# Kernel tuning notes

Measured on AMD Instinct MI355X. Metric: run time of the kernel, lower is better.

Reference implementation:

```python
import jax, jax.numpy as jnp
import numpy as np

BETA = 0.25  # commitment loss weight


def setup_inputs() -> dict:
    key = jax.random.key(0)
    k1, k2 = jax.random.split(key)
    B, D, H, W = 16, 256, 64, 64
    K = 2048  # num_codebook
    z = jax.random.normal(k1, (B, D, H, W), dtype=jnp.float32)
    # matches nn.Embedding init uniform_(-1/K, 1/K) in scale-free way; values irrelevant to math
    codebook = jax.random.uniform(k2, (K, D), dtype=jnp.float32,
                                  minval=-1.0 / K, maxval=1.0 / K)
    return {"z": z, "codebook": codebook}


def reference(z, codebook):
    # z: (B, D, H, W) -> (B, H, W, D) -> (N, D)
    b, d, h, w = z.shape
    k = codebook.shape[0]
    z_flat = jnp.transpose(z, (0, 2, 3, 1)).reshape(-1, d)  # (N, D)

    # squared L2 distance via sum-of-squares + matmul (same expansion as torch code)
    distance = (jnp.sum(z_flat * z_flat, axis=1, keepdims=True)
                + jnp.sum(codebook * codebook, axis=1)
                - 2.0 * jnp.matmul(z_flat, codebook.T))  # (N, K)
    vq_indices = jnp.argmin(distance, axis=1)  # (N,)
    z_quantized = codebook[vq_indices]  # (N, D) gather

    # one-hot counting (scatter-add, equivalent to sum of one-hot)
    vq_current_count = jnp.zeros((k,), dtype=jnp.int32).at[vq_indices].add(1)

    sg = jax.lax.stop_gradient
    codebook_loss = jnp.mean((z_quantized - sg(z_flat)) ** 2)
    commitment_loss = jnp.mean((z_flat - sg(z_quantized)) ** 2)
    loss = codebook_loss + BETA * commitment_loss

    # straight-through estimator
    z_st = z_flat + sg(z_quantized - z_flat)
    q = jnp.transpose(z_st.reshape(b, h, w, d), (0, 3, 1, 2))  # (B, D, H, W)
    return q, loss, codebook_loss, commitment_loss, vq_current_count
```

## Files before the change

kernel.cpp:

```cpp
#include <hip/hip_runtime.h>

#define N_TOT 65536
#define K_CB  2048
#define D_DIM 256
#define HW    4096
#define DHW   1048576

typedef _Float16 half8 __attribute__((ext_vector_type(8)));
typedef _Float16 half4v __attribute__((ext_vector_type(4)));
typedef float f32x16 __attribute__((ext_vector_type(16)));


__device__ __forceinline__ void gload_lds16(const void* g, void* l) {
    __builtin_amdgcn_global_load_lds((const __attribute__((address_space(1))) void*)g,
                                     (__attribute__((address_space(3))) void*)l, 16, 0, 0);
}

__device__ __forceinline__ float pw128_sq(const float* __restrict__ base, int stride) {
    #pragma clang fp contract(off)
    float r[8];
    #pragma unroll
    for (int j = 0; j < 8; ++j) { float v = base[j * stride]; r[j] = v * v; }
    for (int i = 8; i < 128; i += 8) {
        #pragma unroll
        for (int j = 0; j < 8; ++j) { float v = base[(i + j) * stride]; r[j] += v * v; }
    }
    return ((r[0] + r[1]) + (r[2] + r[3])) + ((r[4] + r[5]) + (r[6] + r[7]));
}

__global__ void cbnorm_zero_kernel(const float* __restrict__ cb, float* __restrict__ cb2,
                                   int* __restrict__ counts, float* __restrict__ sse) {
    #pragma clang fp contract(off)
    int k = blockIdx.x * 256 + threadIdx.x;
    const float* row = cb + (size_t)k * D_DIM;
    cb2[k] = pw128_sq(row, 1) + pw128_sq(row + 128, 1);
    counts[k] = 0;
    if (k == 0) *sse = 0.f;
}

__global__ void split_c_kernel(const float* __restrict__ cb,
                               _Float16* __restrict__ ch, _Float16* __restrict__ cl) {
    int e = (blockIdx.x * 256 + threadIdx.x) * 4;
    float4 v = *(const float4*)(cb + e);
    float xs[4] = {v.x, v.y, v.z, v.w};
    half4v hh, hl;
    #pragma unroll
    for (int u = 0; u < 4; ++u) {
        float x = xs[u] * 16384.0f;
        _Float16 hv = (_Float16)x;
        hh[u] = hv;
        hl[u] = (_Float16)(x - (float)hv);
    }
    *(half4v*)(ch + e) = hh;
    *(half4v*)(cl + e) = hl;
}

__global__ void fused_z_kernel(const float* __restrict__ z,
                               _Float16* __restrict__ zh, _Float16* __restrict__ zl,
                               float* __restrict__ z2,
                               unsigned long long* __restrict__ rowmin_g) {
    __shared__ __align__(16) float lt[256 * 33];
    __shared__ float rj[512];
    __shared__ float hh[64];
    int t = threadIdx.x;
    int n0 = blockIdx.x * 32;
    int b = n0 >> 12, s0 = n0 & 4095;
    const float* zb = z + (size_t)b * DHW + s0;

    #pragma unroll
    for (int v = 0; v < 8; ++v) {
        int f = v * 256 + t;
        int d = f >> 3, nch = f & 7;
        float4 val = *(const float4*)(zb + (size_t)d * HW + nch * 4);
        lt[d * 33 + nch * 4 + 0] = val.x;
        lt[d * 33 + nch * 4 + 1] = val.y;
        lt[d * 33 + nch * 4 + 2] = val.z;
        lt[d * 33 + nch * 4 + 3] = val.w;
    }
    __syncthreads();

    {
        #pragma clang fp contract(off)
        int n = t & 31, j = t >> 5;
        #pragma unroll
        for (int hf = 0; hf < 2; ++hf) {
            float r = 0.f;
            #pragma unroll
            for (int i = 0; i < 16; ++i) {
                float v = lt[(hf * 128 + i * 8 + j) * 33 + n];
                r += v * v;
            }
            rj[n * 16 + hf * 8 + j] = r;
        }
    }

    {
        int wv = t >> 6, ln = t & 63;
        int rb = n0 >> 5;
        #pragma unroll
        for (int v = 0; v < 4; ++v) {
            int s = v * 4 + wv;
            int n = ln & 31;
            int d0 = s * 16 + (ln >> 5) * 8;
            half8 hv, lv;
            #pragma unroll
            for (int u = 0; u < 8; ++u) {
                float x = lt[(d0 + u) * 33 + n] * 2048.0f;
                _Float16 h = (_Float16)x;
                hv[u] = h;
                lv[u] = (_Float16)(x - (float)h);
            }
            size_t off = (size_t)rb * 8192 + s * 512 + ln * 8;
            *(half8*)(zh + off) = hv;
            *(half8*)(zl + off) = lv;
        }
    }
    __syncthreads();

    if (t < 64) {
        #pragma clang fp contract(off)
        int n = t & 31, hf = t >> 5;
        const float* r = &rj[n * 16 + hf * 8];
        hh[hf * 32 + n] = ((r[0] + r[1]) + (r[2] + r[3])) + ((r[4] + r[5]) + (r[6] + r[7]));
    }
    __syncthreads();
    if (t < 32) {
        #pragma clang fp contract(off)
        z2[n0 + t] = hh[t] + hh[32 + t];
        rowmin_g[n0 + t] = ~0ull;
    }
}


__device__ __forceinline__ unsigned long long kmin_xor(unsigned long long key, int m) {
    unsigned lo = (unsigned)key, hi = (unsigned)(key >> 32);
    unsigned olo = __shfl_xor(lo, m);
    unsigned ohi = __shfl_xor(hi, m);
    unsigned long long o = ((unsigned long long)ohi << 32) | olo;
    return (o < key) ? o : key;
}

__launch_bounds__(256, 3)
__global__ void argmin_mfma_kernel(const _Float16* __restrict__ zhf, const _Float16* __restrict__ zlf,
                                   const _Float16* __restrict__ ch, const _Float16* __restrict__ cl,
                                   const float* __restrict__ cb2, const float* __restrict__ z2arr,
                                   unsigned long long* __restrict__ rowmin_g) {
    __shared__ __align__(16) char lds_raw[32768];
    _Float16* b0 = (_Float16*)lds_raw;
    _Float16* b1 = (_Float16*)(lds_raw + 16384);

    int t = threadIdx.x;
    int bid = blockIdx.x;
    int swz = (bid & 7) * 1024 + (bid >> 3);
    int r0 = (swz >> 4) * 128;
    int c0 = (swz & 15) * 128;
    int w = t >> 6, lane = t & 63;
    int wm = w >> 1, wn = w & 1;
    int l31 = lane & 31, l5 = lane >> 5;

    f32x16 acc[2][2];
    #pragma unroll
    for (int i = 0; i < 2; ++i)
        #pragma unroll
        for (int j = 0; j < 2; ++j)
            #pragma unroll
            for (int r = 0; r < 16; ++r) acc[i][j][r] = 0.f;

    float c2v[2];
    #pragma unroll
    for (int j = 0; j < 2; ++j)
        c2v[j] = cb2[c0 + wn * 64 + j * 32 + l31];

    size_t abase0 = (size_t)((r0 >> 5) + wm * 2) * 8192 + (size_t)lane * 8;
    size_t abase1 = abase0 + 8192;

    auto stage_B = [&](int kt, _Float16* nb) {
        const _Float16* bsrc = ((kt >> 2) == 1) ? cl : ch;
        int koff = (kt & 3) * 64;
        #pragma unroll
        for (int v = 0; v < 4; ++v) {
            int p = v * 256 + t;
            int row = p >> 3;
            int ku = (p & 7) ^ (row & 7);
            gload_lds16(bsrc + (size_t)((c0 + row) * 256 + koff + ku * 8), nb + p * 8);
        }
    };
    auto load_A = [&](int kt, half8 (&dst)[2][4]) {
        const _Float16* as = (kt < 8) ? zhf : zlf;
        int soff = (kt & 3) * 2048;
        #pragma unroll
        for (int ks = 0; ks < 4; ++ks) {
            dst[0][ks] = *(const half8*)(as + abase0 + soff + ks * 512);
            dst[1][ks] = *(const half8*)(as + abase1 + soff + ks * 512);
        }
    };
    auto compute = [&](const _Float16* lb, const half8 (&af)[2][4]) {
        #pragma unroll
        for (int ks = 0; ks < 4; ++ks) {
            half8 bf[2];
            #pragma unroll
            for (int j = 0; j < 2; ++j) {
                int row = wn * 64 + j * 32 + l31;
                int ku  = (ks * 2 + l5) ^ (row & 7);
                bf[j] = *(const half8*)(lb + row * 64 + ku * 8);
            }
            #pragma unroll
            for (int i = 0; i < 2; ++i)
                #pragma unroll
                for (int j = 0; j < 2; ++j)
                    acc[i][j] = __builtin_amdgcn_mfma_f32_32x32x16_f16(af[i][ks], bf[j], acc[i][j], 0, 0, 0);
        }
    };

    half8 afA[2][4], afB[2][4];

    stage_B(0, b0);
    load_A(0, afA);
    __syncthreads();

    #pragma unroll 1
    for (int kp = 0; kp < 6; ++kp) {
        int kt1 = kp * 2 + 1;
        stage_B(kt1, b1);
        load_A(kt1, afB);
        compute(b0, afA);
        __syncthreads();
        if (kp < 5) {
            stage_B(kt1 + 1, b0);
            load_A(kt1 + 1, afA);
        }
        compute(b1, afB);
        __syncthreads();
    }

    unsigned long long* scratch = (unsigned long long*)lds_raw;
    #pragma unroll
    for (int i = 0; i < 2; ++i) {
        #pragma unroll
        for (int rg = 0; rg < 16; ++rg) {
            int rowoff = (rg & 3) + 8 * (rg >> 2) + 4 * l5;
            int m = wm * 64 + i * 32 + rowoff;
            float zz = z2arr[r0 + m];
            unsigned long long key = ~0ull;
            #pragma unroll
            for (int j = 0; j < 2; ++j) {
                float sc = (zz + c2v[j]) - acc[i][j][rg] * (1.0f / 16777216.0f);
                unsigned long long k2 = ((unsigned long long)__float_as_uint(sc) << 32)
                                      | (unsigned)(c0 + wn * 64 + j * 32 + l31);
                key = (k2 < key) ? k2 : key;
            }
            key = kmin_xor(key, 16);
            key = kmin_xor(key, 8);
            if (l31 < 8) scratch[m * 18 + wn * 8 + l31] = key;
        }
    }
    __syncthreads();
    if (t < 128) {
        const ulonglong2* srow = (const ulonglong2*)(scratch + t * 18);
        unsigned long long best = ~0ull;
        #pragma unroll
        for (int s = 0; s < 8; ++s) {
            ulonglong2 p = srow[s];
            if (p.x < best) best = p.x;
            if (p.y < best) best = p.y;
        }
        atomicMin(&rowmin_g[r0 + t], best);
    }
}

__global__ void gather_kernel(const float* __restrict__ z, const float* __restrict__ cb,
                              const unsigned long long* __restrict__ rowmin_g,
                              float* __restrict__ qout,
                              float* __restrict__ sse, int* __restrict__ counts) {
    __shared__ unsigned long long keys[64];
    __shared__ float red[4];
    int t = threadIdx.x;
    int n0 = blockIdx.x * 64;
    if (t < 64) {
        unsigned long long k = rowmin_g[n0 + t];
        keys[t] = k;
        atomicAdd(&counts[(int)(k & 0xFFFFFFFFull)], 1);
    }
    __syncthreads();

    int sg = (t & 15) * 4;
    int dg = t >> 4;
    int b = n0 >> 12, s0 = (n0 & 4095) + sg;
    const float* zb = z + (size_t)b * DHW + s0;
    float*       qb = qout + (size_t)b * DHW + s0;
    const float* c0p = cb + (size_t)(unsigned)(keys[sg + 0] & 0xFFFFFFFFull) * D_DIM;
    const float* c1p = cb + (size_t)(unsigned)(keys[sg + 1] & 0xFFFFFFFFull) * D_DIM;
    const float* c2p = cb + (size_t)(unsigned)(keys[sg + 2] & 0xFFFFFFFFull) * D_DIM;
    const float* c3p = cb + (size_t)(unsigned)(keys[sg + 3] & 0xFFFFFFFFull) * D_DIM;

    float acc = 0.f;
    #pragma unroll
    for (int dd4 = 0; dd4 < 4; ++dd4) {
        int d = dg * 16 + dd4 * 4;
        float4 cA = *(const float4*)(c0p + d);
        float4 cB = *(const float4*)(c1p + d);
        float4 cC = *(const float4*)(c2p + d);
        float4 cD = *(const float4*)(c3p + d);
        float a0[4] = {cA.x, cA.y, cA.z, cA.w};
        float a1[4] = {cB.x, cB.y, cB.z, cB.w};
        float a2[4] = {cC.x, cC.y, cC.z, cC.w};
        float a3[4] = {cD.x, cD.y, cD.z, cD.w};
        #pragma unroll
        for (int u = 0; u < 4; ++u) {
            float4 zv = *(const float4*)(zb + (size_t)(d + u) * HW);
            float4 qv;
            qv.x = a0[u]; qv.y = a1[u]; qv.z = a2[u]; qv.w = a3[u];
            *(float4*)(qb + (size_t)(d + u) * HW) = qv;
            float e0 = zv.x - qv.x, e1 = zv.y - qv.y;
            float e2 = zv.z - qv.z, e3 = zv.w - qv.w;
            acc += e0 * e0 + e1 * e1 + e2 * e2 + e3 * e3;
        }
    }
    #pragma unroll
    for (int off = 32; off > 0; off >>= 1) acc += __shfl_down(acc, off, 64);
    if ((t & 63) == 0) red[t >> 6] = acc;
    __syncthreads();
    if (t == 0) atomicAdd(sse, (red[0] + red[1]) + (red[2] + red[3]));
}

__global__ void finalize_kernel(const float* __restrict__ sse, const int* __restrict__ counts,
                                float* __restrict__ out) {
    int t = threadIdx.x;
    float mse = *sse * (1.0f / 16777216.0f);
    if (t == 0) {
        out[16777216] = mse * 1.25f;
        out[16777217] = mse;
        out[16777218] = mse;
    }
    for (int i = t; i < 2048; i += 256) out[16777219 + i] = (float)counts[i];
}

extern "C" void kernel_launch(void* const* d_in, const int* in_sizes, int n_in,
                              void* d_out, int out_size, void* d_ws, size_t ws_size,
                              hipStream_t stream) {
    const float* z  = (const float*)d_in[0];
    const float* cb = (const float*)d_in[1];
    float* out = (float*)d_out;
    float* ws  = (float*)d_ws;

    float* cb2    = ws;
    int*   counts = (int*)(ws + 2048);
    float* sse    = ws + 4096;
    float* z2     = ws + 4352;
    unsigned long long* rowmin_g = (unsigned long long*)(ws + 69888);
    _Float16* ch  = (_Float16*)(ws + 200960);
    _Float16* cl  = (_Float16*)(ws + 463104);

    _Float16* zzh = (_Float16*)d_out;
    _Float16* zzl = zzh + 16777216;

    cbnorm_zero_kernel<<<8, 256, 0, stream>>>(cb, cb2, counts, sse);
    split_c_kernel<<<512, 256, 0, stream>>>(cb, ch, cl);
    fused_z_kernel<<<2048, 256, 0, stream>>>(z, zzh, zzl, z2, rowmin_g);
    argmin_mfma_kernel<<<8192, 256, 0, stream>>>(zzh, zzl, ch, cl, cb2, z2, rowmin_g);
    gather_kernel<<<1024, 256, 0, stream>>>(z, cb, rowmin_g, out, sse, counts);
    finalize_kernel<<<1, 256, 0, stream>>>(sse, counts, out);
}
```

Baseline: 419.9 us.

## Enlarge argmin block tile to 256 rows and stream A fragments inline

Each block now covers 256 z rows instead of 128, and each wave owns 64 rows across all 128 codebook columns (2x4 MFMA tiles), so every staged codebook tile in LDS is reused by twice as many rows and the grid is halved. A fragments are no longer prefetched into a double register buffer; they are loaded from global memory inside the compute loop right before use. The LDS scratch reduction is replaced with a full 32-lane shuffle reduction and a per-row atomicMin from a single lane. This cuts codebook traffic and LDS sync overhead, but doubles accumulator registers, which may lower occupancy under the existing launch bounds, and exposes global A-load latency.

Result: slower. 452.1 us (+7.7%).

```diff
diff --git a/kernel.cpp b/kernel.cpp
--- a/kernel.cpp
+++ b/kernel.cpp
@@ -151,27 +151,26 @@
 
     int t = threadIdx.x;
     int bid = blockIdx.x;
-    int swz = (bid & 7) * 1024 + (bid >> 3);
-    int r0 = (swz >> 4) * 128;
+    int swz = (bid & 7) * 512 + (bid >> 3);
+    int r0 = (swz >> 4) * 256;
     int c0 = (swz & 15) * 128;
     int w = t >> 6, lane = t & 63;
-    int wm = w >> 1, wn = w & 1;
     int l31 = lane & 31, l5 = lane >> 5;
 
-    f32x16 acc[2][2];
+    f32x16 acc[2][4];
     #pragma unroll
     for (int i = 0; i < 2; ++i)
         #pragma unroll
-        for (int j = 0; j < 2; ++j)
+        for (int j = 0; j < 4; ++j)
             #pragma unroll
             for (int r = 0; r < 16; ++r) acc[i][j][r] = 0.f;
 
-    float c2v[2];
-    #pragma unroll
-    for (int j = 0; j < 2; ++j)
-        c2v[j] = cb2[c0 + wn * 64 + j * 32 + l31];
-
-    size_t abase0 = (size_t)((r0 >> 5) + wm * 2) * 8192 + (size_t)lane * 8;
+    float c2v[4];
+    #pragma unroll
+    for (int j = 0; j < 4; ++j)
+        c2v[j] = cb2[c0 + j * 32 + l31];
+
+    size_t abase0 = (size_t)((r0 >> 5) + w * 2) * 8192 + (size_t)lane * 8;
     size_t abase1 = abase0 + 8192;
 
     auto stage_B = [&](int kt, _Float16* nb) {
@@ -185,86 +184,61 @@
             gload_lds16(bsrc + (size_t)((c0 + row) * 256 + koff + ku * 8), nb + p * 8);
         }
     };
-    auto load_A = [&](int kt, half8 (&dst)[2][4]) {
+    auto compute = [&](int kt, const _Float16* lb) {
         const _Float16* as = (kt < 8) ? zhf : zlf;
-        int soff = (kt & 3) * 2048;
+        const _Float16* a0p = as + abase0 + (kt & 3) * 2048;
+        const _Float16* a1p = as + abase1 + (kt & 3) * 2048;
         #pragma unroll
         for (int ks = 0; ks < 4; ++ks) {
-            dst[0][ks] = *(const half8*)(as + abase0 + soff + ks * 512);
-            dst[1][ks] = *(const half8*)(as + abase1 + soff + ks * 512);
+            half8 af0 = *(const half8*)(a0p + ks * 512);
+            half8 af1 = *(const half8*)(a1p + ks * 512);
+            #pragma unroll
+            for (int j = 0; j < 4; ++j) {
+                int row = j * 32 + l31;
+                int ku  = (ks * 2 + l5) ^ (row & 7);
+                half8 bf = *(const half8*)(lb + row * 64 + ku * 8);
+                acc[0][j] = __builtin_amdgcn_mfma_f32_32x32x16_f16(af0, bf, acc[0][j], 0, 0, 0);
+                acc[1][j] = __builtin_amdgcn_mfma_f32_32x32x16_f16(af1, bf, acc[1][j], 0, 0, 0);
+            }
         }
     };
-    auto compute = [&](const _Float16* lb, const half8 (&af)[2][4]) {
-        #pragma unroll
-        for (int ks = 0; ks < 4; ++ks) {
-            half8 bf[2];
-            #pragma unroll
-            for (int j = 0; j < 2; ++j) {
-                int row = wn * 64 + j * 32 + l31;
-                int ku  = (ks * 2 + l5) ^ (row & 7);
-                bf[j] = *(const half8*)(lb + row * 64 + ku * 8);
-            }
-            #pragma unroll
-            for (int i = 0; i < 2; ++i)
-                #pragma unroll
-                for (int j = 0; j < 2; ++j)
-                    acc[i][j] = __builtin_amdgcn_mfma_f32_32x32x16_f16(af[i][ks], bf[j], acc[i][j], 0, 0, 0);
-        }
-    };
-
-    half8 afA[2][4], afB[2][4];
 
     stage_B(0, b0);
-    load_A(0, afA);
     __syncthreads();
 
     #pragma unroll 1
     for (int kp = 0; kp < 6; ++kp) {
         int kt1 = kp * 2 + 1;
         stage_B(kt1, b1);
-        load_A(kt1, afB);
-        compute(b0, afA);
+        compute(kp * 2, b0);
         __syncthreads();
-        if (kp < 5) {
-            stage_B(kt1 + 1, b0);
-            load_A(kt1 + 1, afA);
-        }
-        compute(b1, afB);
+        if (kp < 5) stage_B(kt1 + 1, b0);
+        compute(kt1, b1);
         __syncthreads();
     }
 
-    unsigned long long* scratch = (unsigned long long*)lds_raw;
     #pragma unroll
     for (int i = 0; i < 2; ++i) {
         #pragma unroll
         for (int rg = 0; rg < 16; ++rg) {
             int rowoff = (rg & 3) + 8 * (rg >> 2) + 4 * l5;
-            int m = wm * 64 + i * 32 + rowoff;
+            int m = w * 64 + i * 32 + rowoff;
             float zz = z2arr[r0 + m];
             unsigned long long key = ~0ull;
             #pragma unroll
-            for (int j = 0; j < 2; ++j) {
+            for (int j = 0; j < 4; ++j) {
                 float sc = (zz + c2v[j]) - acc[i][j][rg] * (1.0f / 16777216.0f);
                 unsigned long long k2 = ((unsigned long long)__float_as_uint(sc) << 32)
-                                      | (unsigned)(c0 + wn * 64 + j * 32 + l31);
+                                      | (unsigned)(c0 + j * 32 + l31);
                 key = (k2 < key) ? k2 : key;
             }
             key = kmin_xor(key, 16);
             key = kmin_xor(key, 8);
-            if (l31 < 8) scratch[m * 18 + wn * 8 + l31] = key;
-        }
-    }
-    __syncthreads();
-    if (t < 128) {
-        const ulonglong2* srow = (const ulonglong2*)(scratch + t * 18);
-        unsigned long long best = ~0ull;
-        #pragma unroll
-        for (int s = 0; s < 8; ++s) {
-            ulonglong2 p = srow[s];
-            if (p.x < best) best = p.x;
-            if (p.y < best) best = p.y;
-        }
-        atomicMin(&rowmin_g[r0 + t], best);
+            key = kmin_xor(key, 4);
+            key = kmin_xor(key, 2);
+            key = kmin_xor(key, 1);
+            if (l31 == 0) atomicMin(&rowmin_g[r0 + m], key);
+        }
     }
 }
 
@@ -357,7 +331,7 @@
     cbnorm_zero_kernel<<<8, 256, 0, stream>>>(cb, cb2, counts, sse);
     split_c_kernel<<<512, 256, 0, stream>>>(cb, ch, cl);
     fused_z_kernel<<<2048, 256, 0, stream>>>(z, zzh, zzl, z2, rowmin_g);
-    argmin_mfma_kernel<<<8192, 256, 0, stream>>>(zzh, zzl, ch, cl, cb2, z2, rowmin_g);
+    argmin_mfma_kernel<<<4096, 256, 0, stream>>>(zzh, zzl, ch, cl, cb2, z2, rowmin_g);
     gather_kernel<<<1024, 256, 0, stream>>>(z, cb, rowmin_g, out, sse, counts);
     finalize_kernel<<<1, 256, 0, stream>>>(sse, counts, out);
 }
```

## Derive SSE from argmin distance keys and fuse codebook-norm init into split kernel

Applied to the files above, without the earlier changes.

The gather kernel no longer re-reads z to compute the squared error. It sums the minimum distance values already packed in the high 32 bits of each argmin key, accumulating in double. The codebook-norm and zeroing kernel is merged into the codebook split kernel to save one launch. This removes a full 64MB read of z in the gather pass. The risk is that the packed key distance, which comes from fp16-split MFMA arithmetic and may be sign-flipped for ordering, differs from the true fp32 squared error.

Result: no change. 418.4 us (-0.4%).

```diff
diff --git a/kernel.cpp b/kernel.cpp
--- a/kernel.cpp
+++ b/kernel.cpp
@@ -28,18 +28,10 @@
     return ((r[0] + r[1]) + (r[2] + r[3])) + ((r[4] + r[5]) + (r[6] + r[7]));
 }
 
-__global__ void cbnorm_zero_kernel(const float* __restrict__ cb, float* __restrict__ cb2,
-                                   int* __restrict__ counts, float* __restrict__ sse) {
-    #pragma clang fp contract(off)
-    int k = blockIdx.x * 256 + threadIdx.x;
-    const float* row = cb + (size_t)k * D_DIM;
-    cb2[k] = pw128_sq(row, 1) + pw128_sq(row + 128, 1);
-    counts[k] = 0;
-    if (k == 0) *sse = 0.f;
-}
-
 __global__ void split_c_kernel(const float* __restrict__ cb,
-                               _Float16* __restrict__ ch, _Float16* __restrict__ cl) {
+                               _Float16* __restrict__ ch, _Float16* __restrict__ cl,
+                               float* __restrict__ cb2, int* __restrict__ counts,
+                               double* __restrict__ sse) {
     int e = (blockIdx.x * 256 + threadIdx.x) * 4;
     float4 v = *(const float4*)(cb + e);
     float xs[4] = {v.x, v.y, v.z, v.w};
@@ -53,6 +45,14 @@
     }
     *(half4v*)(ch + e) = hh;
     *(half4v*)(cl + e) = hl;
+    if (blockIdx.x < 8) {
+        #pragma clang fp contract(off)
+        int k = blockIdx.x * 256 + threadIdx.x;
+        const float* row = cb + (size_t)k * D_DIM;
+        cb2[k] = pw128_sq(row, 1) + pw128_sq(row + 128, 1);
+        counts[k] = 0;
+        if (k == 0) *sse = 0.0;
+    }
 }
 
 __global__ void fused_z_kernel(const float* __restrict__ z,
@@ -268,32 +268,33 @@
     }
 }
 
-__global__ void gather_kernel(const float* __restrict__ z, const float* __restrict__ cb,
+__global__ void gather_kernel(const float* __restrict__ cb,
                               const unsigned long long* __restrict__ rowmin_g,
                               float* __restrict__ qout,
-                              float* __restrict__ sse, int* __restrict__ counts) {
+                              double* __restrict__ sse, int* __restrict__ counts) {
     __shared__ unsigned long long keys[64];
-    __shared__ float red[4];
     int t = threadIdx.x;
     int n0 = blockIdx.x * 64;
     if (t < 64) {
         unsigned long long k = rowmin_g[n0 + t];
         keys[t] = k;
         atomicAdd(&counts[(int)(k & 0xFFFFFFFFull)], 1);
+        float sc = __uint_as_float((unsigned)(k >> 32));
+        #pragma unroll
+        for (int off = 32; off > 0; off >>= 1) sc += __shfl_down(sc, off, 64);
+        if (t == 0) atomicAdd(sse, (double)sc);
     }
     __syncthreads();
 
     int sg = (t & 15) * 4;
     int dg = t >> 4;
     int b = n0 >> 12, s0 = (n0 & 4095) + sg;
-    const float* zb = z + (size_t)b * DHW + s0;
-    float*       qb = qout + (size_t)b * DHW + s0;
+    float* qb = qout + (size_t)b * DHW + s0;
     const float* c0p = cb + (size_t)(unsigned)(keys[sg + 0] & 0xFFFFFFFFull) * D_DIM;
     const float* c1p = cb + (size_t)(unsigned)(keys[sg + 1] & 0xFFFFFFFFull) * D_DIM;
     const float* c2p = cb + (size_t)(unsigned)(keys[sg + 2] & 0xFFFFFFFFull) * D_DIM;
     const float* c3p = cb + (size_t)(unsigned)(keys[sg + 3] & 0xFFFFFFFFull) * D_DIM;
 
-    float acc = 0.f;
     #pragma unroll
     for (int dd4 = 0; dd4 < 4; ++dd4) {
         int d = dg * 16 + dd4 * 4;
@@ -307,26 +308,17 @@
         float a3[4] = {cD.x, cD.y, cD.z, cD.w};
         #pragma unroll
         for (int u = 0; u < 4; ++u) {
-            float4 zv = *(const float4*)(zb + (size_t)(d + u) * HW);
             float4 qv;
             qv.x = a0[u]; qv.y = a1[u]; qv.z = a2[u]; qv.w = a3[u];
             *(float4*)(qb + (size_t)(d + u) * HW) = qv;
-            float e0 = zv.x - qv.x, e1 = zv.y - qv.y;
-            float e2 = zv.z - qv.z, e3 = zv.w - qv.w;
-            acc += e0 * e0 + e1 * e1 + e2 * e2 + e3 * e3;
-        }
-    }
-    #pragma unroll
-    for (int off = 32; off > 0; off >>= 1) acc += __shfl_down(acc, off, 64);
-    if ((t & 63) == 0) red[t >> 6] = acc;
-    __syncthreads();
-    if (t == 0) atomicAdd(sse, (red[0] + red[1]) + (red[2] + red[3]));
-}
-
-__global__ void finalize_kernel(const float* __restrict__ sse, const int* __restrict__ counts,
+        }
+    }
+}
+
+__global__ void finalize_kernel(const double* __restrict__ sse, const int* __restrict__ counts,
                                 float* __restrict__ out) {
     int t = threadIdx.x;
-    float mse = *sse * (1.0f / 16777216.0f);
+    float mse = (float)(*sse) * (1.0f / 16777216.0f);
     if (t == 0) {
         out[16777216] = mse * 1.25f;
         out[16777217] = mse;
@@ -343,10 +335,10 @@
     float* out = (float*)d_out;
     float* ws  = (float*)d_ws;
 
-    float* cb2    = ws;
-    int*   counts = (int*)(ws + 2048);
-    float* sse    = ws + 4096;
-    float* z2     = ws + 4352;
+    float*  cb2    = ws;
+    int*    counts = (int*)(ws + 2048);
+    double* sse    = (double*)(ws + 4096);
+    float*  z2     = ws + 4352;
     unsigned long long* rowmin_g = (unsigned long long*)(ws + 69888);
     _Float16* ch  = (_Float16*)(ws + 200960);
     _Float16* cl  = (_Float16*)(ws + 463104);
@@ -354,10 +346,9 @@
     _Float16* zzh = (_Float16*)d_out;
     _Float16* zzl = zzh + 16777216;
 
-    cbnorm_zero_kernel<<<8, 256, 0, stream>>>(cb, cb2, counts, sse);
-    split_c_kernel<<<512, 256, 0, stream>>>(cb, ch, cl);
+    split_c_kernel<<<512, 256, 0, stream>>>(cb, ch, cl, cb2, counts, sse);
     fused_z_kernel<<<2048, 256, 0, stream>>>(z, zzh, zzl, z2, rowmin_g);
     argmin_mfma_kernel<<<8192, 256, 0, stream>>>(zzh, zzl, ch, cl, cb2, z2, rowmin_g);
-    gather_kernel<<<1024, 256, 0, stream>>>(z, cb, rowmin_g, out, sse, counts);
+    gather_kernel<<<1024, 256, 0, stream>>>(cb, rowmin_g, out, sse, counts);
     finalize_kernel<<<1, 256, 0, stream>>>(sse, counts, out);
 }
```
